# Performance work log

Measured on AMD Instinct MI355X. Metric: run time of the kernel, lower is better.

## Reference

```python
import jax, jax.numpy as jnp
import numpy as np

B, C, W, H = 32, 64, 96, 96
L = 32          # LSTM hidden size
OUT = 256       # conv output channels
EPS = 1e-5


def _lstm_dir(x, wih, whh, b):
    # x: [N, T, D]; wih: [4L, D]; whh: [4L, L]; b: [4L] (b_ih + b_hh)
    N, T, D = x.shape
    Lh = whh.shape[1]
    xg = jnp.einsum('ntd,gd->ntg', x, wih) + b  # precompute input projections

    def step(carry, xg_t):
        h, c = carry
        g = xg_t + h @ whh.T
        i, f, gg, o = jnp.split(g, 4, axis=-1)  # PyTorch gate order i,f,g,o
        i = jax.nn.sigmoid(i)
        f = jax.nn.sigmoid(f)
        gg = jnp.tanh(gg)
        o = jax.nn.sigmoid(o)
        c = f * c + i * gg
        h = o * jnp.tanh(c)
        return (h, c), h

    init = (jnp.zeros((N, Lh), x.dtype), jnp.zeros((N, Lh), x.dtype))
    _, hs = jax.lax.scan(step, init, jnp.swapaxes(xg, 0, 1))
    return jnp.swapaxes(hs, 0, 1)  # [N, T, L]


def _bilstm(x, wih_f, whh_f, bih_f, bhh_f, wih_b, whh_b, bih_b, bhh_b):
    hf = _lstm_dir(x, wih_f, whh_f, bih_f + bhh_f)
    hb = _lstm_dir(x[:, ::-1], wih_b, whh_b, bih_b + bhh_b)[:, ::-1]
    return jnp.concatenate([hf, hb], axis=-1)  # [N, T, 2L]


def setup_inputs() -> dict:
    key = jax.random.key(0)
    ks = jax.random.split(key, 24)
    s1 = 1.0 / np.sqrt(L)
    def u(k, shape):
        return jax.random.uniform(k, shape, jnp.float32, -s1, s1)
    inp = {'x': jax.random.normal(ks[0], (B, C, W, H), jnp.float32)}
    # vertical LSTM: input_size=C
    inp['v_wih_f'] = u(ks[1], (4 * L, C)); inp['v_whh_f'] = u(ks[2], (4 * L, L))
    inp['v_bih_f'] = u(ks[3], (4 * L,));  inp['v_bhh_f'] = u(ks[4], (4 * L,))
    inp['v_wih_b'] = u(ks[5], (4 * L, C)); inp['v_whh_b'] = u(ks[6], (4 * L, L))
    inp['v_bih_b'] = u(ks[7], (4 * L,));  inp['v_bhh_b'] = u(ks[8], (4 * L,))
    # horizontal LSTM: input_size=2L
    inp['h_wih_f'] = u(ks[9], (4 * L, 2 * L)); inp['h_whh_f'] = u(ks[10], (4 * L, L))
    inp['h_bih_f'] = u(ks[11], (4 * L,));      inp['h_bhh_f'] = u(ks[12], (4 * L,))
    inp['h_wih_b'] = u(ks[13], (4 * L, 2 * L)); inp['h_whh_b'] = u(ks[14], (4 * L, L))
    inp['h_bih_b'] = u(ks[15], (4 * L,));       inp['h_bhh_b'] = u(ks[16], (4 * L,))
    # 1x1 conv + BN
    inp['conv_w'] = jax.random.normal(ks[17], (OUT, 2 * L), jnp.float32) * 0.05
    inp['conv_b'] = jnp.zeros((OUT,), jnp.float32)
    inp['bn_g'] = jnp.ones((OUT,), jnp.float32)
    inp['bn_b'] = jnp.zeros((OUT,), jnp.float32)
    return inp


def reference(x, v_wih_f, v_whh_f, v_bih_f, v_bhh_f, v_wih_b, v_whh_b, v_bih_b, v_bhh_b,
              h_wih_f, h_whh_f, h_bih_f, h_bhh_f, h_wih_b, h_whh_b, h_bih_b, h_bhh_b,
              conv_w, conv_b, bn_g, bn_b):
    b, c, w, h = x.shape
    xt = jnp.transpose(x, (0, 3, 2, 1))  # [B, H, W, C] (torch transpose(1,3))
    # vertical pass: for each column w, LSTM over H -> batch all columns at once
    xv = jnp.transpose(xt, (0, 2, 1, 3)).reshape(b * w, h, c)  # [B*W, H, C]
    hv = _bilstm(xv, v_wih_f, v_whh_f, v_bih_f, v_bhh_f,
                 v_wih_b, v_whh_b, v_bih_b, v_bhh_b)            # [B*W, H, 2L]
    v = jnp.transpose(hv.reshape(b, w, h, 2 * L), (0, 2, 1, 3))  # [B, H, W, 2L]
    # horizontal pass: for each row h, LSTM over W -> batch all rows at once
    xh = v.reshape(b * h, w, 2 * L)
    hh = _bilstm(xh, h_wih_f, h_whh_f, h_bih_f, h_bhh_f,
                 h_wih_b, h_whh_b, h_bih_b, h_bhh_b).reshape(b, h, w, 2 * L)
    # stack(dim=3) then transpose(1,2) in torch == [B, 2L, W, H]
    y = jnp.transpose(hh, (0, 3, 2, 1))  # [B, 2L, W, H]
    # 1x1 conv
    y = jnp.einsum('bcwh,oc->bowh', y, conv_w) + conv_b[None, :, None, None]
    # BatchNorm2d (training mode: batch statistics, biased variance)
    mean = jnp.mean(y, axis=(0, 2, 3), keepdims=True)
    var = jnp.mean((y - mean) ** 2, axis=(0, 2, 3), keepdims=True)
    out = (y - mean) * jax.lax.rsqrt(var + EPS)
    out = out * bn_g[None, :, None, None] + bn_b[None, :, None, None]
    return out
```

## Files before the change

kernel.cpp:

```cpp
#include <hip/hip_runtime.h>
#include <stdint.h>

#define DI __device__ __forceinline__

constexpr int Bn = 32, Cc = 64, Wn = 96, Hn = 96, Ln = 32, NG = 128, OUTC = 256;
constexpr int SEQ = 96;
constexpr long long NPIX = (long long)Bn * Wn * Hn;
constexpr int GRAM_BLOCKS = 256;
constexpr int PIX_PER_BLOCK = (int)(NPIX / GRAM_BLOCKS);

typedef __attribute__((ext_vector_type(8))) short bf16x8;
typedef __attribute__((ext_vector_type(4))) float f32x4;

constexpr float LOG2E  = 1.44269504088896340736f;
constexpr float TWOL2E = 2.88539008177792681472f;

DI float exp2_(float x) { return __builtin_amdgcn_exp2f(x); }
DI float rcp_(float x)  { return __builtin_amdgcn_rcpf(x); }
DI float bf2f(unsigned short u) { return __uint_as_float(((unsigned)u) << 16); }
DI unsigned short f2bf(float f) {
    unsigned u = __float_as_uint(f);
    u += 0x7FFFu + ((u >> 16) & 1u);
    return (unsigned short)(u >> 16);
}

union U32x4 { unsigned u[4]; bf16x8 v; };

__global__ __launch_bounds__(256)
void transpose_x(const float* __restrict__ x, unsigned short* __restrict__ xT)
{
    __shared__ alignas(16) unsigned char xs[96 * 128];
    const int tid = threadIdx.x;
    const int b = blockIdx.x / 96, q = blockIdx.x % 96;
    for (int i = tid; i < 1536; i += 256) {
        int c = i / 24, h4 = i - c * 24;
        float4 v = *(const float4*)(x + (((size_t)b * 64 + c) * 96 + q) * 96 + 4 * h4);
        float vv[4] = {v.x, v.y, v.z, v.w};
#pragma unroll
        for (int j = 0; j < 4; ++j) {
            int h = 4 * h4 + j;
            *(unsigned short*)(xs + h * 128 + ((c * 2) ^ ((h & 7) << 4))) = f2bf(vv[j]);
        }
    }
    __syncthreads();
    unsigned short* ob = xT + (size_t)blockIdx.x * 6144;
    for (int i = tid; i < 768; i += 256) {
        int row = i >> 3, k8 = i & 7;
        bf16x8 p = *(const bf16x8*)(xs + row * 128 + ((k8 * 16) ^ ((row & 7) << 4)));
        *(bf16x8*)(ob + (size_t)i * 8) = p;
    }
}

#define FLOAD(XA, XB, STI)                                                     \
    if ((STI) < 96) {                                                          \
        const int tl_ = dir ? 95 - (STI) : (STI);                              \
        XA = *(const bf16x8*)(xTb + (size_t)tl_ * 64);                         \
        XB = *(const bf16x8*)(xTb + (size_t)tl_ * 64 + 32);                    \
    }

#define PPROJ(XA, XB)                                                          \
    _Pragma("unroll")                                                          \
    for (int tt = 0; tt < 8; ++tt) {                                           \
        f32x4 tp_ = __builtin_amdgcn_mfma_f32_16x16x32_bf16(ax0[tt], XA, bc[tt], 0, 0, 0); \
        xac[tt] = __builtin_amdgcn_mfma_f32_16x16x32_bf16(ax1[tt], XB, tp_, 0, 0, 0);      \
    }

#define RSTEP(STI)                                                             \
    {                                                                          \
        U32x4 hu;                                                              \
        {                                                                      \
            int a0 = __shfl((int)pk0x, srcL0), a1 = __shfl((int)pk0y, srcL0);  \
            int a2 = __shfl((int)pk0x, srcL1), a3 = __shfl((int)pk0y, srcL1);  \
            int b0 = __shfl((int)pk1x, srcL0), b1 = __shfl((int)pk1y, srcL0);  \
            int b2 = __shfl((int)pk1x, srcL1), b3 = __shfl((int)pk1y, srcL1);  \
            hu.u[0] = sp ? (unsigned)b0 : (unsigned)a0;                        \
            hu.u[1] = sp ? (unsigned)b1 : (unsigned)a1;                        \
            hu.u[2] = sp ? (unsigned)b2 : (unsigned)a2;                        \
            hu.u[3] = sp ? (unsigned)b3 : (unsigned)a3;                        \
        }                                                                      \
        f32x4 ac_[8];                                                          \
        _Pragma("unroll")                                                      \
        for (int tt = 0; tt < 8; ++tt)                                         \
            ac_[tt] = __builtin_amdgcn_mfma_f32_16x16x32_bf16(ah[tt], hu.v, xac[tt], 0, 0, 0); \
        _Pragma("unroll")                                                      \
        for (int s = 0; s < 2; ++s) {                                          \
            unsigned short hs[4];                                              \
            _Pragma("unroll")                                                  \
            for (int j = 0; j < 4; ++j) {                                      \
                const float iv = rcp_(1.f + exp2_(-ac_[0 + s][j]));            \
                const float fv = rcp_(1.f + exp2_(-ac_[2 + s][j]));            \
                const float gr = rcp_(1.f + exp2_(-ac_[4 + s][j]));            \
                const float gv = fmaf(2.f, gr, -1.f);                          \
                const float ov = rcp_(1.f + exp2_(-ac_[6 + s][j]));            \
                cc[s][j] = fmaf(fv, cc[s][j], iv * gv);                        \
                const float r_ = rcp_(exp2_(cc[s][j] * TWOL2E) + 1.f);         \
                const float t2 = -2.f * ov;                                    \
                hs[j] = f2bf(fmaf(t2, r_, ov));                                \
            }                                                                  \
            const unsigned dlo = ((unsigned)hs[1] << 16) | hs[0];              \
            const unsigned dhi = ((unsigned)hs[3] << 16) | hs[2];              \
            if (s == 0) { pk0x = dlo; pk0y = dhi; } else { pk1x = dlo; pk1y = dhi; } \
            ushort4 hp; hp.x = hs[0]; hp.y = hs[1]; hp.z = hs[2]; hp.w = hs[3];\
            *(ushort4*)(optr + s * 16) = hp;                                   \
        }                                                                      \
        optr += odelta;                                                        \
    }

template<int VERT>
__global__ __launch_bounds__(64, 1)
void lstm_fused(const unsigned short* __restrict__ xT,
                const float* __restrict__ wih_f, const float* __restrict__ whh_f,
                const float* __restrict__ bih_f, const float* __restrict__ bhh_f,
                const float* __restrict__ wih_b, const float* __restrict__ whh_b,
                const float* __restrict__ bih_b, const float* __restrict__ bhh_b,
                unsigned short* __restrict__ outU)
{
    const int lane = threadIdx.x;
    const int dir = blockIdx.x & 1, group = blockIdx.x >> 1;
    const int n_ = lane & 15, rg = lane >> 4;
    const int chain = group * 16 + n_;
    const int b = group / 6;
    const int q = (group % 6) * 16 + n_;

    const float* wih = dir ? wih_b : wih_f;
    const float* whh = dir ? whh_b : whh_f;
    const float* bih = dir ? bih_b : bih_f;
    const float* bhh = dir ? bhh_b : bhh_f;

    bf16x8 ah[8], ax0[8], ax1[8];
    f32x4 bc[8];
#pragma unroll
    for (int tt = 0; tt < 8; ++tt) {
        const float sc = (tt == 4 || tt == 5) ? TWOL2E : LOG2E;
        const float* sh = whh + (size_t)(tt * 16 + n_) * 32 + rg * 8;
        const float* sx = wih + (size_t)(tt * 16 + n_) * 64 + rg * 8;
        float4 h0 = *(const float4*)sh, h1 = *(const float4*)(sh + 4);
        float4 x0 = *(const float4*)sx, x1 = *(const float4*)(sx + 4);
        float4 x2 = *(const float4*)(sx + 32), x3 = *(const float4*)(sx + 36);
        ah[tt][0] = (short)f2bf(sc * h0.x); ah[tt][1] = (short)f2bf(sc * h0.y);
        ah[tt][2] = (short)f2bf(sc * h0.z); ah[tt][3] = (short)f2bf(sc * h0.w);
        ah[tt][4] = (short)f2bf(sc * h1.x); ah[tt][5] = (short)f2bf(sc * h1.y);
        ah[tt][6] = (short)f2bf(sc * h1.z); ah[tt][7] = (short)f2bf(sc * h1.w);
        ax0[tt][0] = (short)f2bf(sc * x0.x); ax0[tt][1] = (short)f2bf(sc * x0.y);
        ax0[tt][2] = (short)f2bf(sc * x0.z); ax0[tt][3] = (short)f2bf(sc * x0.w);
        ax0[tt][4] = (short)f2bf(sc * x1.x); ax0[tt][5] = (short)f2bf(sc * x1.y);
        ax0[tt][6] = (short)f2bf(sc * x1.z); ax0[tt][7] = (short)f2bf(sc * x1.w);
        ax1[tt][0] = (short)f2bf(sc * x2.x); ax1[tt][1] = (short)f2bf(sc * x2.y);
        ax1[tt][2] = (short)f2bf(sc * x2.z); ax1[tt][3] = (short)f2bf(sc * x2.w);
        ax1[tt][4] = (short)f2bf(sc * x3.x); ax1[tt][5] = (short)f2bf(sc * x3.y);
        ax1[tt][6] = (short)f2bf(sc * x3.z); ax1[tt][7] = (short)f2bf(sc * x3.w);
#pragma unroll
        for (int j = 0; j < 4; ++j) {
            const int g = tt * 16 + rg * 4 + j;
            bc[tt][j] = sc * (bih[g] + bhh[g]);
        }
    }

    const int sp = rg >> 1;
    const int srcL0 = ((rg & 1) << 1) * 16 + n_;
    const int srcL1 = srcL0 + 16;

    const unsigned short* xTb = xT + (size_t)chain * 6144 + rg * 8;

    const int t0 = dir ? 95 : 0;
    const size_t o0 = VERT ? ((((size_t)b * 96 + t0) * 96 + q) * 64)
                           : ((((size_t)b * 96 + q) * 96 + t0) * 64);
    unsigned short* optr = outU + o0 + dir * 32 + rg * 4;
    const ptrdiff_t odelta = (ptrdiff_t)(dir ? -1 : 1) * (VERT ? 6144 : 64);

    unsigned pk0x = 0, pk0y = 0, pk1x = 0, pk1y = 0;
    float cc[2][4];
#pragma unroll
    for (int s = 0; s < 2; ++s)
#pragma unroll
        for (int j = 0; j < 4; ++j) cc[s][j] = 0.f;

    f32x4 xac[8];
    bf16x8 xa0, xb0, xa1, xb1, xa2, xb2;
    FLOAD(xa0, xb0, 0)
    FLOAD(xa1, xb1, 1)
    PPROJ(xa0, xb0)

    for (int st = 0; st < 96; st += 3) {
        FLOAD(xa2, xb2, st + 2)
        RSTEP(st)
        PPROJ(xa1, xb1)
        FLOAD(xa0, xb0, st + 3)
        RSTEP(st + 1)
        PPROJ(xa2, xb2)
        FLOAD(xa1, xb1, st + 4)
        RSTEP(st + 2)
        PPROJ(xa0, xb0)
    }
}

__global__ __launch_bounds__(256, 2)
void gram_partial(const unsigned short* __restrict__ hh, float* __restrict__ part)
{
    __shared__ alignas(16) unsigned char xsT[2][64 * 144];
    __shared__ float sumb[16][64];

    const int tid = threadIdx.x;
    const int wv = tid >> 6, lane = tid & 63;
    const int lrow = lane & 15, lkg = lane >> 4;
    const int cq = tid & 15, pr = tid >> 4;

    float csum[4] = {0.f, 0.f, 0.f, 0.f};
    f32x4 acc[4];
#pragma unroll
    for (int n = 0; n < 4; ++n) acc[n] = (f32x4){0.f, 0.f, 0.f, 0.f};

    const size_t pix0 = (size_t)blockIdx.x * PIX_PER_BLOCK;

    for (int tile = 0; tile < PIX_PER_BLOCK / 64; ++tile) {
        unsigned char* Xb = xsT[tile & 1];
#pragma unroll
        for (int r = 0; r < 4; ++r) {
            const int p = pr + r * 16;
            ushort4 v = *(const ushort4*)(hh + (pix0 + (size_t)tile * 64 + p) * 64 + cq * 4);
            csum[0] += bf2f(v.x); csum[1] += bf2f(v.y);
            csum[2] += bf2f(v.z); csum[3] += bf2f(v.w);
            *(unsigned short*)(Xb + (cq * 4 + 0) * 144 + p * 2) = v.x;
            *(unsigned short*)(Xb + (cq * 4 + 1) * 144 + p * 2) = v.y;
            *(unsigned short*)(Xb + (cq * 4 + 2) * 144 + p * 2) = v.z;
            *(unsigned short*)(Xb + (cq * 4 + 3) * 144 + p * 2) = v.w;
        }
        __syncthreads();
#pragma unroll
        for (int kc = 0; kc < 2; ++kc) {
            const int kb = (kc * 32 + lkg * 8) * 2;
            bf16x8 af = *(const bf16x8*)(Xb + (wv * 16 + lrow) * 144 + kb);
#pragma unroll
            for (int n = 0; n < 4; ++n) {
                bf16x8 bf_ = *(const bf16x8*)(Xb + (n * 16 + lrow) * 144 + kb);
                acc[n] = __builtin_amdgcn_mfma_f32_16x16x32_bf16(af, bf_, acc[n], 0, 0, 0);
            }
        }
    }

    *(float4*)&sumb[pr][cq * 4] = (float4){csum[0], csum[1], csum[2], csum[3]};
    __syncthreads();
    float* pb = part + (size_t)blockIdx.x * 4160;
    if (tid < 64) {
        float s = 0.f;
#pragma unroll
        for (int r = 0; r < 16; ++r) s += sumb[r][tid];
        pb[4096 + tid] = s;
    }
#pragma unroll
    for (int n = 0; n < 4; ++n)
#pragma unroll
        for (int r = 0; r < 4; ++r)
            pb[(wv * 16 + lkg * 4 + r) * 64 + n * 16 + lrow] = acc[n][r];
}

__global__ void gram_reduce(const float* __restrict__ part, float* __restrict__ M)
{
    int e = blockIdx.x * 256 + threadIdx.x;
    if (e >= 4160) return;
    double s = 0.0;
    for (int p = 0; p < GRAM_BLOCKS; ++p) s += (double)part[(size_t)p * 4160 + e];
    M[e] = (float)s;
}

__global__ __launch_bounds__(256)
void stats_kernel(const float* __restrict__ M, const float* __restrict__ cw,
                  const float* __restrict__ cb, const float* __restrict__ bg,
                  const float* __restrict__ bb,
                  float* __restrict__ Aout, float* __restrict__ Bout)
{
    __shared__ float Ml[4160];
    const int tid = threadIdx.x;
    for (int e = tid; e < 4160; e += 256) Ml[e] = M[e];
    __syncthreads();
    float wr[64];
#pragma unroll
    for (int c = 0; c < 64; ++c) wr[c] = bf2f(f2bf(cw[tid * 64 + c]));
    float s1 = 0.f;
#pragma unroll
    for (int c = 0; c < 64; ++c) s1 = fmaf(wr[c], Ml[4096 + c], s1);
    float s2 = 0.f;
    for (int c = 0; c < 64; ++c) {
        const float* Mr = &Ml[c * 64];
        float t = 0.f;
#pragma unroll
        for (int d = 0; d < 64; ++d) t = fmaf(wr[d], Mr[d], t);
        s2 = fmaf(wr[c], t, s2);
    }
    const double invN = 1.0 / (double)NPIX;
    double cbo = (double)cb[tid];
    double mu = (double)s1 * invN + cbo;
    double ey2 = (double)s2 * invN + 2.0 * cbo * ((double)s1 * invN) + cbo * cbo;
    double var = ey2 - mu * mu;
    double A = (double)bg[tid] / sqrt(var + 1e-5);
    Aout[tid] = (float)A;
    Bout[tid] = (float)((double)bb[tid] + A * (cbo - mu));
}

__global__ __launch_bounds__(512, 2)
void conv_bn_kernel(const unsigned short* __restrict__ hh, const float* __restrict__ cw,
                    const float* __restrict__ Aarr, const float* __restrict__ Barr,
                    float* __restrict__ out)
{
    __shared__ alignas(16) unsigned char UsB[96 * 128];
    __shared__ alignas(16) unsigned char WtB[256 * 128];

    const int tid = threadIdx.x;
    const int b = blockIdx.x / 96, w = blockIdx.x % 96;

    for (int i4 = tid; i4 < 4096; i4 += 512) {
        int wrow = i4 >> 4, k4 = i4 & 15;
        float4 v = *(const float4*)(cw + (size_t)wrow * 64 + k4 * 4);
        ushort4 p; p.x = f2bf(v.x); p.y = f2bf(v.y); p.z = f2bf(v.z); p.w = f2bf(v.w);
        *(ushort4*)(WtB + wrow * 128 + ((k4 * 8) ^ ((wrow & 7) << 4))) = p;
    }
    for (int i = tid; i < 1536; i += 512) {
        int row = i >> 4, k4 = i & 15;
        ushort4 p = *(const ushort4*)(hh + (((size_t)b * 96 + row) * 96 + w) * 64 + k4 * 4);
        *(ushort4*)(UsB + row * 128 + ((k4 * 8) ^ ((row & 7) << 4))) = p;
    }
    __syncthreads();

    const int wv = tid >> 6, lane = tid & 63;
    const int mbase = (wv >> 2) * 48, nbase = (wv & 3) * 64;
    const int lrow = lane & 15, lk = (lane >> 4) * 8;

    f32x4 acc[3][4];
#pragma unroll
    for (int m = 0; m < 3; ++m)
#pragma unroll
        for (int n = 0; n < 4; ++n)
            acc[m][n] = (f32x4){0.f, 0.f, 0.f, 0.f};

#pragma unroll
    for (int ks = 0; ks < 2; ++ks) {
        const int kb = (ks * 32 + lk) * 2;
        bf16x8 am[3], bn[4];
#pragma unroll
        for (int m = 0; m < 3; ++m) {
            int row = mbase + m * 16 + lrow;
            am[m] = *(const bf16x8*)(UsB + row * 128 + (kb ^ ((row & 7) << 4)));
        }
#pragma unroll
        for (int n = 0; n < 4; ++n) {
            int o = nbase + n * 16 + lrow;
            bn[n] = *(const bf16x8*)(WtB + o * 128 + (kb ^ ((o & 7) << 4)));
        }
#pragma unroll
        for (int m = 0; m < 3; ++m)
#pragma unroll
            for (int n = 0; n < 4; ++n)
                acc[m][n] = __builtin_amdgcn_mfma_f32_16x16x32_bf16(am[m], bn[n], acc[m][n], 0, 0, 0);
    }

    const int hbase0 = (lane >> 4) * 4;
#pragma unroll
    for (int n = 0; n < 4; ++n) {
        const int o = nbase + n * 16 + lrow;
        const float Ao = Aarr[o], Bo = Barr[o];
        float* obase = out + (((size_t)b * 256 + o) * 96 + w) * 96;
#pragma unroll
        for (int m = 0; m < 3; ++m) {
            const int h0 = mbase + m * 16 + hbase0;
            f32x4 res;
            res[0] = fmaf(Ao, acc[m][n][0], Bo);
            res[1] = fmaf(Ao, acc[m][n][1], Bo);
            res[2] = fmaf(Ao, acc[m][n][2], Bo);
            res[3] = fmaf(Ao, acc[m][n][3], Bo);
            __builtin_nontemporal_store(res, (f32x4*)(obase + h0));
        }
    }
}

extern "C" void kernel_launch(void* const* d_in, const int* in_sizes, int n_in,
                              void* d_out, int out_size, void* d_ws, size_t ws_size,
                              hipStream_t stream)
{
    const float* x       = (const float*)d_in[0];
    const float* v_wih_f = (const float*)d_in[1];
    const float* v_whh_f = (const float*)d_in[2];
    const float* v_bih_f = (const float*)d_in[3];
    const float* v_bhh_f = (const float*)d_in[4];
    const float* v_wih_b = (const float*)d_in[5];
    const float* v_whh_b = (const float*)d_in[6];
    const float* v_bih_b = (const float*)d_in[7];
    const float* v_bhh_b = (const float*)d_in[8];
    const float* h_wih_f = (const float*)d_in[9];
    const float* h_whh_f = (const float*)d_in[10];
    const float* h_bih_f = (const float*)d_in[11];
    const float* h_bhh_f = (const float*)d_in[12];
    const float* h_wih_b = (const float*)d_in[13];
    const float* h_whh_b = (const float*)d_in[14];
    const float* h_bih_b = (const float*)d_in[15];
    const float* h_bhh_b = (const float*)d_in[16];
    const float* conv_w  = (const float*)d_in[17];
    const float* conv_b  = (const float*)d_in[18];
    const float* bn_g    = (const float*)d_in[19];
    const float* bn_b    = (const float*)d_in[20];
    float* out = (float*)d_out;

    const size_t v_elems = (size_t)Bn * Hn * Wn * 64;
    unsigned short* v_buf = (unsigned short*)(out + (size_t)out_size) - v_elems;
    unsigned short* xT = (unsigned short*)d_out;
    float* part = (float*)((char*)d_out + (64u << 20));

    unsigned short* hh = (unsigned short*)d_ws;
    char* wsb = (char*)d_ws;
    float* M    = (float*)(wsb + 37748736);
    float* Aarr = M + 4160;
    float* Barr = Aarr + 256;

    transpose_x<<<3072, 256, 0, stream>>>(x, xT);
    lstm_fused<1><<<384, 64, 0, stream>>>(xT, v_wih_f, v_whh_f, v_bih_f, v_bhh_f,
                                          v_wih_b, v_whh_b, v_bih_b, v_bhh_b, v_buf);
    lstm_fused<0><<<384, 64, 0, stream>>>(v_buf, h_wih_f, h_whh_f, h_bih_f, h_bhh_f,
                                          h_wih_b, h_whh_b, h_bih_b, h_bhh_b, hh);
    gram_partial<<<GRAM_BLOCKS, 256, 0, stream>>>(hh, part);
    gram_reduce<<<17, 256, 0, stream>>>(part, M);
    stats_kernel<<<1, 256, 0, stream>>>(M, conv_w, conv_b, bn_g, bn_b, Aarr, Barr);
    conv_bn_kernel<<<3072, 512, 0, stream>>>(hh, conv_w, Aarr, Barr, out);
}
```

Before: 347.3 us.

## Split LSTM recurrence across two waves with LDS hidden-state exchange

Each LSTM block now runs two wavefronts instead of one. Each wave computes half of the hidden units (one 16-row tile per gate) and the pair exchanges the new hidden state through a double-buffered shared-memory array with a barrier every timestep, replacing the cross-lane shuffles. This halves the per-wave MFMA and transcendental work on the serial critical path and raises parallelism, since only 384 single-wave blocks ran before. In exchange it adds a block barrier and LDS round trip to every one of the 96 steps.

Result: faster. 339.2 us (-2.3%).

```diff
diff --git a/kernel.cpp b/kernel.cpp
--- a/kernel.cpp
+++ b/kernel.cpp
@@ -24,8 +24,6 @@
     return (unsigned short)(u >> 16);
 }
 
-union U32x4 { unsigned u[4]; bf16x8 v; };
-
 __global__ __launch_bounds__(256)
 void transpose_x(const float* __restrict__ x, unsigned short* __restrict__ xT)
 {
@@ -60,54 +58,41 @@
 
 #define PPROJ(XA, XB)                                                          \
     _Pragma("unroll")                                                          \
-    for (int tt = 0; tt < 8; ++tt) {                                           \
-        f32x4 tp_ = __builtin_amdgcn_mfma_f32_16x16x32_bf16(ax0[tt], XA, bc[tt], 0, 0, 0); \
-        xac[tt] = __builtin_amdgcn_mfma_f32_16x16x32_bf16(ax1[tt], XB, tp_, 0, 0, 0);      \
+    for (int g_ = 0; g_ < 4; ++g_) {                                           \
+        f32x4 tp_ = __builtin_amdgcn_mfma_f32_16x16x32_bf16(ax0[g_], XA, bc[g_], 0, 0, 0); \
+        xac[g_] = __builtin_amdgcn_mfma_f32_16x16x32_bf16(ax1[g_], XB, tp_, 0, 0, 0);      \
     }
 
 #define RSTEP(STI)                                                             \
     {                                                                          \
-        U32x4 hu;                                                              \
-        {                                                                      \
-            int a0 = __shfl((int)pk0x, srcL0), a1 = __shfl((int)pk0y, srcL0);  \
-            int a2 = __shfl((int)pk0x, srcL1), a3 = __shfl((int)pk0y, srcL1);  \
-            int b0 = __shfl((int)pk1x, srcL0), b1 = __shfl((int)pk1y, srcL0);  \
-            int b2 = __shfl((int)pk1x, srcL1), b3 = __shfl((int)pk1y, srcL1);  \
-            hu.u[0] = sp ? (unsigned)b0 : (unsigned)a0;                        \
-            hu.u[1] = sp ? (unsigned)b1 : (unsigned)a1;                        \
-            hu.u[2] = sp ? (unsigned)b2 : (unsigned)a2;                        \
-            hu.u[3] = sp ? (unsigned)b3 : (unsigned)a3;                        \
+        const bf16x8 hu = *(const bf16x8*)(hcur + n_ * 80 + rg * 16);          \
+        f32x4 ac_[4];                                                          \
+        _Pragma("unroll")                                                      \
+        for (int g_ = 0; g_ < 4; ++g_)                                         \
+            ac_[g_] = __builtin_amdgcn_mfma_f32_16x16x32_bf16(ah[g_], hu, xac[g_], 0, 0, 0); \
+        unsigned short hs[4];                                                  \
+        _Pragma("unroll")                                                      \
+        for (int j = 0; j < 4; ++j) {                                          \
+            const float iv = rcp_(1.f + exp2_(-ac_[0][j]));                    \
+            const float fv = rcp_(1.f + exp2_(-ac_[1][j]));                    \
+            const float gr = rcp_(1.f + exp2_(-ac_[2][j]));                    \
+            const float gv = fmaf(2.f, gr, -1.f);                              \
+            const float ov = rcp_(1.f + exp2_(-ac_[3][j]));                    \
+            cc[j] = fmaf(fv, cc[j], iv * gv);                                  \
+            const float r_ = rcp_(exp2_(cc[j] * TWOL2E) + 1.f);                \
+            const float t2 = -2.f * ov;                                        \
+            hs[j] = f2bf(fmaf(t2, r_, ov));                                    \
         }                                                                      \
-        f32x4 ac_[8];                                                          \
-        _Pragma("unroll")                                                      \
-        for (int tt = 0; tt < 8; ++tt)                                         \
-            ac_[tt] = __builtin_amdgcn_mfma_f32_16x16x32_bf16(ah[tt], hu.v, xac[tt], 0, 0, 0); \
-        _Pragma("unroll")                                                      \
-        for (int s = 0; s < 2; ++s) {                                          \
-            unsigned short hs[4];                                              \
-            _Pragma("unroll")                                                  \
-            for (int j = 0; j < 4; ++j) {                                      \
-                const float iv = rcp_(1.f + exp2_(-ac_[0 + s][j]));            \
-                const float fv = rcp_(1.f + exp2_(-ac_[2 + s][j]));            \
-                const float gr = rcp_(1.f + exp2_(-ac_[4 + s][j]));            \
-                const float gv = fmaf(2.f, gr, -1.f);                          \
-                const float ov = rcp_(1.f + exp2_(-ac_[6 + s][j]));            \
-                cc[s][j] = fmaf(fv, cc[s][j], iv * gv);                        \
-                const float r_ = rcp_(exp2_(cc[s][j] * TWOL2E) + 1.f);         \
-                const float t2 = -2.f * ov;                                    \
-                hs[j] = f2bf(fmaf(t2, r_, ov));                                \
-            }                                                                  \
-            const unsigned dlo = ((unsigned)hs[1] << 16) | hs[0];              \
-            const unsigned dhi = ((unsigned)hs[3] << 16) | hs[2];              \
-            if (s == 0) { pk0x = dlo; pk0y = dhi; } else { pk1x = dlo; pk1y = dhi; } \
-            ushort4 hp; hp.x = hs[0]; hp.y = hs[1]; hp.z = hs[2]; hp.w = hs[3];\
-            *(ushort4*)(optr + s * 16) = hp;                                   \
-        }                                                                      \
+        ushort4 hp; hp.x = hs[0]; hp.y = hs[1]; hp.z = hs[2]; hp.w = hs[3];    \
+        *(ushort4*)(hnxt + n_ * 80 + wv * 32 + rg * 8) = hp;                   \
+        *(ushort4*)optr = hp;                                                  \
         optr += odelta;                                                        \
+        __syncthreads();                                                       \
+        { unsigned char* t_ = hcur; hcur = hnxt; hnxt = t_; }                  \
     }
 
 template<int VERT>
-__global__ __launch_bounds__(64, 1)
+__global__ __launch_bounds__(128, 1)
 void lstm_fused(const unsigned short* __restrict__ xT,
                 const float* __restrict__ wih_f, const float* __restrict__ whh_f,
                 const float* __restrict__ bih_f, const float* __restrict__ bhh_f,
@@ -115,7 +100,10 @@
                 const float* __restrict__ bih_b, const float* __restrict__ bhh_b,
                 unsigned short* __restrict__ outU)
 {
-    const int lane = threadIdx.x;
+    __shared__ alignas(16) unsigned char hbuf[2][16 * 80];
+
+    const int tid = threadIdx.x;
+    const int wv = tid >> 6, lane = tid & 63;
     const int dir = blockIdx.x & 1, group = blockIdx.x >> 1;
     const int n_ = lane & 15, rg = lane >> 4;
     const int chain = group * 16 + n_;
@@ -127,59 +115,56 @@
     const float* bih = dir ? bih_b : bih_f;
     const float* bhh = dir ? bhh_b : bhh_f;
 
-    bf16x8 ah[8], ax0[8], ax1[8];
-    f32x4 bc[8];
-#pragma unroll
-    for (int tt = 0; tt < 8; ++tt) {
-        const float sc = (tt == 4 || tt == 5) ? TWOL2E : LOG2E;
+    bf16x8 ah[4], ax0[4], ax1[4];
+    f32x4 bc[4];
+#pragma unroll
+    for (int g_ = 0; g_ < 4; ++g_) {
+        const int tt = 2 * g_ + wv;
+        const float sc = (g_ == 2) ? TWOL2E : LOG2E;
         const float* sh = whh + (size_t)(tt * 16 + n_) * 32 + rg * 8;
         const float* sx = wih + (size_t)(tt * 16 + n_) * 64 + rg * 8;
         float4 h0 = *(const float4*)sh, h1 = *(const float4*)(sh + 4);
         float4 x0 = *(const float4*)sx, x1 = *(const float4*)(sx + 4);
         float4 x2 = *(const float4*)(sx + 32), x3 = *(const float4*)(sx + 36);
-        ah[tt][0] = (short)f2bf(sc * h0.x); ah[tt][1] = (short)f2bf(sc * h0.y);
-        ah[tt][2] = (short)f2bf(sc * h0.z); ah[tt][3] = (short)f2bf(sc * h0.w);
-        ah[tt][4] = (short)f2bf(sc * h1.x); ah[tt][5] = (short)f2bf(sc * h1.y);
-        ah[tt][6] = (short)f2bf(sc * h1.z); ah[tt][7] = (short)f2bf(sc * h1.w);
-        ax0[tt][0] = (short)f2bf(sc * x0.x); ax0[tt][1] = (short)f2bf(sc * x0.y);
-        ax0[tt][2] = (short)f2bf(sc * x0.z); ax0[tt][3] = (short)f2bf(sc * x0.w);
-        ax0[tt][4] = (short)f2bf(sc * x1.x); ax0[tt][5] = (short)f2bf(sc * x1.y);
-        ax0[tt][6] = (short)f2bf(sc * x1.z); ax0[tt][7] = (short)f2bf(sc * x1.w);
-        ax1[tt][0] = (short)f2bf(sc * x2.x); ax1[tt][1] = (short)f2bf(sc * x2.y);
-        ax1[tt][2] = (short)f2bf(sc * x2.z); ax1[tt][3] = (short)f2bf(sc * x2.w);
-        ax1[tt][4] = (short)f2bf(sc * x3.x); ax1[tt][5] = (short)f2bf(sc * x3.y);
-        ax1[tt][6] = (short)f2bf(sc * x3.z); ax1[tt][7] = (short)f2bf(sc * x3.w);
+        ah[g_][0] = (short)f2bf(sc * h0.x); ah[g_][1] = (short)f2bf(sc * h0.y);
+        ah[g_][2] = (short)f2bf(sc * h0.z); ah[g_][3] = (short)f2bf(sc * h0.w);
+        ah[g_][4] = (short)f2bf(sc * h1.x); ah[g_][5] = (short)f2bf(sc * h1.y);
+        ah[g_][6] = (short)f2bf(sc * h1.z); ah[g_][7] = (short)f2bf(sc * h1.w);
+        ax0[g_][0] = (short)f2bf(sc * x0.x); ax0[g_][1] = (short)f2bf(sc * x0.y);
+        ax0[g_][2] = (short)f2bf(sc * x0.z); ax0[g_][3] = (short)f2bf(sc * x0.w);
+        ax0[g_][4] = (short)f2bf(sc * x1.x); ax0[g_][5] = (short)f2bf(sc * x1.y);
+        ax0[g_][6] = (short)f2bf(sc * x1.z); ax0[g_][7] = (short)f2bf(sc * x1.w);
+        ax1[g_][0] = (short)f2bf(sc * x2.x); ax1[g_][1] = (short)f2bf(sc * x2.y);
+        ax1[g_][2] = (short)f2bf(sc * x2.z); ax1[g_][3] = (short)f2bf(sc * x2.w);
+        ax1[g_][4] = (short)f2bf(sc * x3.x); ax1[g_][5] = (short)f2bf(sc * x3.y);
+        ax1[g_][6] = (short)f2bf(sc * x3.z); ax1[g_][7] = (short)f2bf(sc * x3.w);
 #pragma unroll
         for (int j = 0; j < 4; ++j) {
             const int g = tt * 16 + rg * 4 + j;
-            bc[tt][j] = sc * (bih[g] + bhh[g]);
-        }
-    }
-
-    const int sp = rg >> 1;
-    const int srcL0 = ((rg & 1) << 1) * 16 + n_;
-    const int srcL1 = srcL0 + 16;
+            bc[g_][j] = sc * (bih[g] + bhh[g]);
+        }
+    }
 
     const unsigned short* xTb = xT + (size_t)chain * 6144 + rg * 8;
 
     const int t0 = dir ? 95 : 0;
     const size_t o0 = VERT ? ((((size_t)b * 96 + t0) * 96 + q) * 64)
                            : ((((size_t)b * 96 + q) * 96 + t0) * 64);
-    unsigned short* optr = outU + o0 + dir * 32 + rg * 4;
+    unsigned short* optr = outU + o0 + dir * 32 + wv * 16 + rg * 4;
     const ptrdiff_t odelta = (ptrdiff_t)(dir ? -1 : 1) * (VERT ? 6144 : 64);
 
-    unsigned pk0x = 0, pk0y = 0, pk1x = 0, pk1y = 0;
-    float cc[2][4];
-#pragma unroll
-    for (int s = 0; s < 2; ++s)
-#pragma unroll
-        for (int j = 0; j < 4; ++j) cc[s][j] = 0.f;
-
-    f32x4 xac[8];
+    for (int i = tid; i < 320; i += 128) ((unsigned*)hbuf[0])[i] = 0u;
+
+    unsigned char* hcur = hbuf[0];
+    unsigned char* hnxt = hbuf[1];
+
+    float cc[4] = {0.f, 0.f, 0.f, 0.f};
+    f32x4 xac[4];
     bf16x8 xa0, xb0, xa1, xb1, xa2, xb2;
     FLOAD(xa0, xb0, 0)
     FLOAD(xa1, xb1, 1)
     PPROJ(xa0, xb0)
+    __syncthreads();
 
     for (int st = 0; st < 96; st += 3) {
         FLOAD(xa2, xb2, st + 2)
@@ -411,10 +396,10 @@
     float* Barr = Aarr + 256;
 
     transpose_x<<<3072, 256, 0, stream>>>(x, xT);
-    lstm_fused<1><<<384, 64, 0, stream>>>(xT, v_wih_f, v_whh_f, v_bih_f, v_bhh_f,
-                                          v_wih_b, v_whh_b, v_bih_b, v_bhh_b, v_buf);
-    lstm_fused<0><<<384, 64, 0, stream>>>(v_buf, h_wih_f, h_whh_f, h_bih_f, h_bhh_f,
-                                          h_wih_b, h_whh_b, h_bih_b, h_bhh_b, hh);
+    lstm_fused<1><<<384, 128, 0, stream>>>(xT, v_wih_f, v_whh_f, v_bih_f, v_bhh_f,
+                                           v_wih_b, v_whh_b, v_bih_b, v_bhh_b, v_buf);
+    lstm_fused<0><<<384, 128, 0, stream>>>(v_buf, h_wih_f, h_whh_f, h_bih_f, h_bhh_f,
+                                           h_wih_b, h_whh_b, h_bih_b, h_bhh_b, hh);
     gram_partial<<<GRAM_BLOCKS, 256, 0, stream>>>(hh, part);
     gram_reduce<<<17, 256, 0, stream>>>(part, M);
     stats_kernel<<<1, 256, 0, stream>>>(M, conv_w, conv_b, bn_g, bn_b, Aarr, Barr);
```
